# Performance work log

Measured on AMD Instinct MI355X. Metric: run time of the kernel, lower is better.

## Reference

```python
import jax, jax.numpy as jnp
import numpy as np

B, T, C = 8, 2048, 1024
H = 4 * C
N_LAYER, LAYER_ID = 12, 2
K_CLAMP = 60.0
LN_EPS = 1e-5


def _ln(x, g, b):
    m = jnp.mean(x, axis=-1, keepdims=True)
    v = jnp.var(x, axis=-1, keepdims=True)
    return (x - m) * jax.lax.rsqrt(v + LN_EPS) * g + b


def _mix(x, time_mix, combined_mix):
    # x: (B,T,C). Causal shift (zeros at t=0), anti-causal shift (zeros at t=T-1).
    c = x.shape[-1]
    xm1 = jnp.pad(x[:, :-1], ((0, 0), (1, 0), (0, 0)))
    xp1 = jnp.pad(x[:, 1:], ((0, 0), (0, 1), (0, 0)))
    xc = jnp.concatenate([xm1[..., :c // 2], xp1[..., c // 2:]], axis=-1)
    return x * time_mix + xm1 * (1.0 - time_mix) + xc * combined_mix


def _wkv(time_decay, time_first, k, v):
    # RWKV WKV exponential-decay linear recurrence (the custom CUDA kernel).
    # k, v: (B,T,C); k > 0 (already clamped+exp'd).
    # y_t = (a_t + exp(u)*k_t*v_t) / (b_t + exp(u)*k_t)
    # a_{t+1} = exp(-exp(w))*a_t + k_t*v_t ; b likewise with v=1.
    ed = jnp.exp(-jnp.exp(time_decay))  # per-step channel decay, (C,)
    eu = jnp.exp(time_first)            # current-token bonus, (C,)

    def step(carry, kv_t):
        a, b = carry
        kt, vt = kv_t
        y = (a + eu * kt * vt) / (b + eu * kt)
        return (ed * a + kt * vt, ed * b + kt), y

    kT = jnp.swapaxes(k, 0, 1)  # (T,B,C)
    vT = jnp.swapaxes(v, 0, 1)
    z = jnp.zeros_like(kT[0])
    _, y = jax.lax.scan(step, (z, z), (kT, vT))
    return jnp.swapaxes(y, 0, 1)  # (B,T,C)


def _time_mix_block(x, time_mix, combined_mix, time_decay, time_first, Wk, Wv, Wr, Wo):
    xm = _mix(x, time_mix, combined_mix)
    k = jnp.exp(jnp.minimum(xm @ Wk.T, K_CLAMP))
    v = xm @ Wv.T
    r = xm @ Wr.T
    wkv = _wkv(time_decay, time_first, k, v)
    return (jax.nn.sigmoid(r) * wkv) @ Wo.T


def _channel_mix_block(x, time_mix, combined_mix, Fk, Fv, Fr):
    xm = _mix(x, time_mix, combined_mix)
    k = jnp.square(jax.nn.relu(xm @ Fk.T))
    kv = k @ Fv.T
    return jax.nn.sigmoid(xm @ Fr.T) * kv


def setup_inputs():
    key = jax.random.key(0)
    ks = jax.random.split(key, 9)
    s = 0.02
    x = jax.random.normal(ks[0], (B, T, C), jnp.float32)
    # time_decay init per the module (f1/f2 interpolation over layers)
    h = np.arange(C, dtype=np.float64)
    frac = (LAYER_ID - 1) / (N_LAYER - 2)
    f1 = 3.0 + frac * (1.2 - 3.0)
    f2 = 0.65 + frac * (0.4 - 0.65)
    decay_speed = np.power(f2, h / (C - 1) * 7.0) * f1
    tm = jnp.concatenate([jnp.zeros(C // 2), jnp.ones(C // 2)]).reshape(1, 1, C).astype(jnp.float32)
    return dict(
        x=x,
        ln1_g=jnp.ones((C,), jnp.float32), ln1_b=jnp.zeros((C,), jnp.float32),
        ln2_g=jnp.ones((C,), jnp.float32), ln2_b=jnp.zeros((C,), jnp.float32),
        att_time_mix=tm,
        att_combined_mix=jnp.full((1, 1, C), 0.01, jnp.float32),
        time_decay=jnp.asarray(np.log(decay_speed), jnp.float32),
        time_first=jnp.full((C,), float(np.log(0.3)), jnp.float32),
        Wk=jax.random.normal(ks[1], (C, C), jnp.float32) * s,
        Wv=jax.random.normal(ks[2], (C, C), jnp.float32) * s,
        Wr=jax.random.normal(ks[3], (C, C), jnp.float32) * s,
        Wo=jax.random.normal(ks[4], (C, C), jnp.float32) * s,
        ffn_time_mix=tm,
        ffn_combined_mix=jnp.full((1, 1, C), 0.01, jnp.float32),
        Fk=jax.random.normal(ks[5], (H, C), jnp.float32) * s,
        Fv=jax.random.normal(ks[6], (C, H), jnp.float32) * s,
        Fr=jax.random.normal(ks[7], (C, C), jnp.float32) * s,
    )


def reference(x, ln1_g, ln1_b, ln2_g, ln2_b, att_time_mix, att_combined_mix,
              time_decay, time_first, Wk, Wv, Wr, Wo,
              ffn_time_mix, ffn_combined_mix, Fk, Fv, Fr):
    x = _ln(x, ln1_g, ln1_b)
    x = x + _time_mix_block(x, att_time_mix, att_combined_mix, time_decay, time_first, Wk, Wv, Wr, Wo)
    x = _ln(x, ln2_g, ln2_b)
    x = x + _channel_mix_block(x, ffn_time_mix, ffn_combined_mix, Fk, Fv, Fr)
    return x
```

## Files before the change

### kernel.cpp

```cpp
#include <hip/hip_runtime.h>
#include <hip/hip_bf16.h>

typedef float f32x4 __attribute__((ext_vector_type(4)));
typedef __bf16 bf16x8 __attribute__((ext_vector_type(8)));
typedef __bf16 bf16x4 __attribute__((ext_vector_type(4)));

#define DEVI static __device__ __forceinline__

DEVI void glds16(const void* g, void* l) {
  __builtin_amdgcn_global_load_lds((__attribute__((address_space(1))) void*)g,
                                   (__attribute__((address_space(3))) void*)l, 16, 0, 0);
}

DEVI f32x4 load4(const float* p) { return *(const f32x4*)p; }
DEVI f32x4 load4(const __bf16* p) {
  bf16x4 v = *(const bf16x4*)p;
  f32x4 o = { (float)v[0], (float)v[1], (float)v[2], (float)v[3] };
  return o;
}
DEVI void store4(float* p, f32x4 v) { *(f32x4*)p = v; }
DEVI void store4(__bf16* p, f32x4 v) {
  bf16x4 o = { (__bf16)v[0], (__bf16)v[1], (__bf16)v[2], (__bf16)v[3] };
  *(bf16x4*)p = o;
}

__global__ void cvt_bf16(const float* __restrict__ in, __bf16* __restrict__ out, int n4) {
  int i = blockIdx.x * 256 + threadIdx.x;
  if (i < n4) {
    f32x4 v = *(const f32x4*)(in + (size_t)i * 4);
    store4(out + (size_t)i * 4, v);
  }
}

template <typename TIN, typename TOUT>
__global__ __launch_bounds__(256) void ln_kernel(const TIN* __restrict__ x,
    const float* __restrict__ gw, const float* __restrict__ bw,
    TOUT* __restrict__ out) {
  const size_t row = blockIdx.x;
  f32x4 v = load4(x + row * 1024 + threadIdx.x * 4);
  float s = v[0] + v[1] + v[2] + v[3];
  float q = v[0]*v[0] + v[1]*v[1] + v[2]*v[2] + v[3]*v[3];
#pragma unroll
  for (int o = 32; o > 0; o >>= 1) { s += __shfl_down(s, o); q += __shfl_down(q, o); }
  __shared__ float ss[4], qq[4];
  const int w = threadIdx.x >> 6, l = threadIdx.x & 63;
  if (l == 0) { ss[w] = s; qq[w] = q; }
  __syncthreads();
  s = ss[0] + ss[1] + ss[2] + ss[3];
  q = qq[0] + qq[1] + qq[2] + qq[3];
  const float mean = s * (1.0f / 1024.0f);
  const float var = q * (1.0f / 1024.0f) - mean * mean;
  const float rstd = rsqrtf(var + 1e-5f);
  f32x4 g4 = *(const f32x4*)(gw + threadIdx.x * 4);
  f32x4 b4 = *(const f32x4*)(bw + threadIdx.x * 4);
  f32x4 o;
#pragma unroll
  for (int j = 0; j < 4; ++j) o[j] = (v[j] - mean) * rstd * g4[j] + b4[j];
  store4(out + row * 1024 + threadIdx.x * 4, o);
}

template <typename TIN>
__global__ __launch_bounds__(256) void mix_kernel(const TIN* __restrict__ x,
    const float* __restrict__ tm, const float* __restrict__ cm,
    __bf16* __restrict__ out) {
  const int idx = blockIdx.x * 256 + threadIdx.x;
  const int t = (idx >> 8) & 2047;
  const int c = (idx & 255) * 4;
  const size_t base = ((size_t)(idx >> 8) << 10) + c;
  f32x4 xv = load4(x + base);
  f32x4 xm1 = {0.f, 0.f, 0.f, 0.f}, xp1 = {0.f, 0.f, 0.f, 0.f};
  if (t > 0)    xm1 = load4(x + base - 1024);
  if (t < 2047) xp1 = load4(x + base + 1024);
  f32x4 tm4 = *(const f32x4*)(tm + c);
  f32x4 cm4 = *(const f32x4*)(cm + c);
  f32x4 xc = (c < 512) ? xm1 : xp1;
  f32x4 o;
#pragma unroll
  for (int j = 0; j < 4; ++j)
    o[j] = xv[j] * tm4[j] + xm1[j] * (1.0f - tm4[j]) + xc[j] * cm4[j];
  store4(out + base, o);
}

__global__ __launch_bounds__(256) void wkv_part(const __bf16* __restrict__ k,
    const __bf16* __restrict__ v, const float* __restrict__ td,
    float* __restrict__ scA, float* __restrict__ scB) {
  const int gid = blockIdx.x * 256 + threadIdx.x;
  const int c = gid & 1023;
  const int j = (gid >> 10) & 31;
  const int b = gid >> 15;
  const float ed = expf(-expf(td[c]));
  float A = 0.f, Bv = 0.f;
  size_t off = ((size_t)(b * 2048 + j * 64) << 10) + c;
#pragma unroll 4
  for (int i = 0; i < 64; ++i, off += 1024) {
    const float kt = (float)k[off];
    const float kv = kt * (float)v[off];
    A = ed * A + kv;
    Bv = ed * Bv + kt;
  }
  scA[gid] = A;
  scB[gid] = Bv;
}

__global__ __launch_bounds__(256) void wkv_scan(const float* __restrict__ td,
    float* __restrict__ scA, float* __restrict__ scB) {
  const int gid = blockIdx.x * 256 + threadIdx.x;
  const int c = gid & 1023;
  const int b = gid >> 10;
  const float edL = expf(-expf(td[c]) * 64.0f);
  float a = 0.f, bb = 0.f;
  size_t off = ((size_t)b << 15) + c;
  for (int j = 0; j < 32; ++j, off += 1024) {
    const float Aj = scA[off], Bj = scB[off];
    scA[off] = a;
    scB[off] = bb;
    a = edL * a + Aj;
    bb = edL * bb + Bj;
  }
}

__global__ __launch_bounds__(256) void wkv_apply(const __bf16* __restrict__ k,
    const __bf16* __restrict__ v, const __bf16* __restrict__ sr,
    const float* __restrict__ td, const float* __restrict__ tf,
    const float* __restrict__ scA, const float* __restrict__ scB,
    __bf16* __restrict__ srw) {
  const int gid = blockIdx.x * 256 + threadIdx.x;
  const int c = gid & 1023;
  const int j = (gid >> 10) & 31;
  const int b = gid >> 15;
  const float ed = expf(-expf(td[c]));
  const float eu = expf(tf[c]);
  float a = scA[gid], bb = scB[gid];
  size_t off = ((size_t)(b * 2048 + j * 64) << 10) + c;
#pragma unroll 4
  for (int i = 0; i < 64; ++i, off += 1024) {
    const float kt = (float)k[off];
    const float vt = (float)v[off];
    const float kv = kt * vt;
    const float y = (a + eu * kv) / (bb + eu * kt);
    srw[off] = (__bf16)((float)sr[off] * y);
    a = ed * a + kv;
    bb = ed * bb + kt;
  }
}

enum { EPI_NONE = 0, EPI_EXP, EPI_SIG, EPI_RELU2, EPI_RESID, EPI_FINAL, EPI_KVR };

#define SBAR() { __builtin_amdgcn_s_barrier(); __builtin_amdgcn_sched_barrier(0); }
#define WAITL0() { asm volatile("s_waitcnt lgkmcnt(0)" ::: "memory"); __builtin_amdgcn_sched_barrier(0); }
#define VMW(n) { asm volatile("s_waitcnt vmcnt(" #n ")" ::: "memory"); __builtin_amdgcn_sched_barrier(0); }

template <int EPI>
__global__ __launch_bounds__(512, 2) void gemm8p(
    const __bf16* __restrict__ A, const __bf16* __restrict__ W,
    void* outp, const void* res, const void* sig, const int N, const int K) {
  __shared__ __bf16 sA[2][16384];
  __shared__ __bf16 sB[2][16384];
  const int tid = threadIdx.x;
  const int w = tid >> 6, l = tid & 63;
  const int wm = w >> 2, wn = w & 3;

  const int nwg = gridDim.x * gridDim.y;
  int wg = blockIdx.y * gridDim.x + blockIdx.x;
  wg = (wg & 7) * (nwg >> 3) + (wg >> 3);
  const int m0 = (wg / gridDim.x) << 8;
  const int n0 = (wg % gridDim.x) << 8;

  const int lr = l >> 3;
  const int lc = (l & 7) ^ lr;
  const size_t gA = (size_t)(m0 + w * 8 + lr) * K + lc * 8;
  const size_t gB = (size_t)(n0 + wn * 64 + wm * 8 + lr) * K + lc * 8;
  const int ldsA = w * 512;
  const int ldsB = (wn * 64 + wm * 8) * 64;

  const int NTK = K >> 6;

#define STAGE_A(buf, kt, i) glds16(A + gA + (size_t)(i) * 64 * K + (size_t)(kt) * 64, &sA[buf][ldsA + (i) * 4096])
#define STAGE_B(buf, kt, j) glds16(W + gB + (size_t)(j) * 16 * K + (size_t)(kt) * 64, &sB[buf][ldsB + (j) * 1024])

  const int rA = (wm * 128 + (l & 15)) * 64;
  const int rB = (wn * 64 + (l & 15)) * 64;
  const int csw = l & 7;
  const int k0 = l >> 4;
#define LDA(buf, mi, kk) (*(const bf16x8*)&sA[buf][rA + (mi) * 1024 + ((((kk) * 4 + k0) ^ csw) << 3)])
#define LDB(buf, ni, kk) (*(const bf16x8*)&sB[buf][rB + (ni) * 1024 + ((((kk) * 4 + k0) ^ csw) << 3)])

  f32x4 acc[8][4] = {};
  bf16x8 afr[8], b0[4], b1[4];

  STAGE_B(0, 0, 0); STAGE_B(0, 0, 1); STAGE_A(0, 0, 0); STAGE_A(0, 0, 2);
  STAGE_B(0, 0, 2); STAGE_B(0, 0, 3); STAGE_A(0, 0, 1); STAGE_A(0, 0, 3);

  for (int kt = 0; kt < NTK; ++kt) {
    const int buf = kt & 1, nb = buf ^ 1;
    const bool st = (kt + 1 < NTK);
    VMW(4); SBAR();
#pragma unroll
    for (int mi = 0; mi < 4; ++mi) {
      afr[mi * 2 + 0] = LDA(buf, mi, 0);
      afr[mi * 2 + 1] = LDA(buf, mi, 1);
    }
#pragma unroll
    for (int ni = 0; ni < 2; ++ni) {
      b0[ni * 2 + 0] = LDB(buf, ni, 0);
      b0[ni * 2 + 1] = LDB(buf, ni, 1);
    }
    if (st) { STAGE_B(nb, kt + 1, 0); STAGE_B(nb, kt + 1, 1); }
    WAITL0();
    __builtin_amdgcn_s_setprio(1);
#pragma unroll
    for (int mi = 0; mi < 4; ++mi)
#pragma unroll
      for (int ni = 0; ni < 2; ++ni)
#pragma unroll
        for (int kk = 0; kk < 2; ++kk)
          acc[mi][ni] = __builtin_amdgcn_mfma_f32_16x16x32_bf16(afr[mi*2+kk], b0[ni*2+kk], acc[mi][ni], 0, 0, 0);
    __builtin_amdgcn_s_setprio(0);
    if (st) { VMW(4); } else { VMW(2); }
    SBAR();
#pragma unroll
    for (int ni = 0; ni < 2; ++ni) {
      b1[ni * 2 + 0] = LDB(buf, ni + 2, 0);
      b1[ni * 2 + 1] = LDB(buf, ni + 2, 1);
    }
    if (st) { STAGE_A(nb, kt + 1, 0); STAGE_A(nb, kt + 1, 2); }
    WAITL0();
    __builtin_amdgcn_s_setprio(1);
#pragma unroll
    for (int mi = 0; mi < 4; ++mi)
#pragma unroll
      for (int ni = 0; ni < 2; ++ni)
#pragma unroll
        for (int kk = 0; kk < 2; ++kk)
          acc[mi][ni + 2] = __builtin_amdgcn_mfma_f32_16x16x32_bf16(afr[mi*2+kk], b1[ni*2+kk], acc[mi][ni + 2], 0, 0, 0);
    __builtin_amdgcn_s_setprio(0);
    if (st) { VMW(4); } else { VMW(0); }
    SBAR();
#pragma unroll
    for (int mi = 0; mi < 4; ++mi) {
      afr[mi * 2 + 0] = LDA(buf, mi + 4, 0);
      afr[mi * 2 + 1] = LDA(buf, mi + 4, 1);
    }
    if (st) { STAGE_B(nb, kt + 1, 2); STAGE_B(nb, kt + 1, 3); }
    WAITL0();
    __builtin_amdgcn_s_setprio(1);
#pragma unroll
    for (int mi = 0; mi < 4; ++mi)
#pragma unroll
      for (int ni = 0; ni < 2; ++ni)
#pragma unroll
        for (int kk = 0; kk < 2; ++kk)
          acc[mi + 4][ni] = __builtin_amdgcn_mfma_f32_16x16x32_bf16(afr[mi*2+kk], b0[ni*2+kk], acc[mi + 4][ni], 0, 0, 0);
    __builtin_amdgcn_s_setprio(0);
    if (st) { STAGE_A(nb, kt + 1, 1); STAGE_A(nb, kt + 1, 3); }
    __builtin_amdgcn_s_setprio(1);
#pragma unroll
    for (int mi = 0; mi < 4; ++mi)
#pragma unroll
      for (int ni = 0; ni < 2; ++ni)
#pragma unroll
        for (int kk = 0; kk < 2; ++kk)
          acc[mi + 4][ni + 2] = __builtin_amdgcn_mfma_f32_16x16x32_bf16(afr[mi*2+kk], b1[ni*2+kk], acc[mi + 4][ni + 2], 0, 0, 0);
    __builtin_amdgcn_s_setprio(0);
  }

  const int rl = (l >> 4) << 2, cl = l & 15;
#pragma unroll
  for (int mi = 0; mi < 8; ++mi) {
#pragma unroll
    for (int ni = 0; ni < 4; ++ni) {
#pragma unroll
      for (int e = 0; e < 4; ++e) {
        const int r = m0 + (wm << 7) + mi * 16 + rl + e;
        const int cidx = n0 + (wn << 6) + ni * 16 + cl;
        const size_t idx = (size_t)r * N + cidx;
        const float vacc = acc[mi][ni][e];
        if constexpr (EPI == EPI_NONE) {
          ((__bf16*)outp)[idx] = (__bf16)vacc;
        } else if constexpr (EPI == EPI_EXP) {
          ((__bf16*)outp)[idx] = (__bf16)expf(fminf(vacc, 60.0f));
        } else if constexpr (EPI == EPI_SIG) {
          ((__bf16*)outp)[idx] = (__bf16)(1.0f / (1.0f + expf(-vacc)));
        } else if constexpr (EPI == EPI_RELU2) {
          const float rv = fmaxf(vacc, 0.0f);
          ((__bf16*)outp)[idx] = (__bf16)(rv * rv);
        } else if constexpr (EPI == EPI_RESID) {
          ((__bf16*)outp)[idx] = (__bf16)(vacc + (float)((const __bf16*)res)[idx]);
        } else if constexpr (EPI == EPI_FINAL) {
          ((float*)outp)[idx] = ((const float*)res)[idx] + (float)((const __bf16*)sig)[idx] * vacc;
        } else {
          const int sel = cidx >> 10;
          const size_t oidx = (size_t)r * 1024 + (cidx & 1023);
          if (sel == 0)      ((__bf16*)outp)[oidx] = (__bf16)expf(fminf(vacc, 60.0f));
          else if (sel == 1) ((__bf16*)const_cast<void*>(res))[oidx] = (__bf16)vacc;
          else               ((__bf16*)const_cast<void*>(sig))[oidx] = (__bf16)(1.0f / (1.0f + expf(-vacc)));
        }
      }
    }
  }
}

extern "C" void kernel_launch(void* const* d_in, const int* in_sizes, int n_in,
                              void* d_out, int out_size, void* d_ws, size_t ws_size,
                              hipStream_t stream) {
  (void)in_sizes; (void)n_in; (void)out_size;
  const float* x    = (const float*)d_in[0];
  const float* ln1g = (const float*)d_in[1];
  const float* ln1b = (const float*)d_in[2];
  const float* ln2g = (const float*)d_in[3];
  const float* ln2b = (const float*)d_in[4];
  const float* atm  = (const float*)d_in[5];
  const float* acm  = (const float*)d_in[6];
  const float* td   = (const float*)d_in[7];
  const float* tf   = (const float*)d_in[8];
  const float* Wk   = (const float*)d_in[9];
  const float* Wv   = (const float*)d_in[10];
  const float* Wr   = (const float*)d_in[11];
  const float* Wo   = (const float*)d_in[12];
  const float* ftm  = (const float*)d_in[13];
  const float* fcm  = (const float*)d_in[14];
  const float* Fk   = (const float*)d_in[15];
  const float* Fv   = (const float*)d_in[16];
  const float* Fr   = (const float*)d_in[17];

  constexpr size_t C = 1024, T = 2048, Bs = 8, H = 4096;
  constexpr size_t NT = Bs * T;
  constexpr size_t NTC = NT * C;
  constexpr size_t CC = C * C;
  constexpr size_t CH = C * H;

  char* p = (char*)d_ws;
  auto takeb = [&](size_t elems) { __bf16* q = (__bf16*)p; p += elems * 2; return q; };
  __bf16* wKVR = takeb(3 * CC);
  __bf16* wWo  = takeb(CC);
  __bf16* wFk  = takeb(CH);
  __bf16* wFv  = takeb(CH);
  __bf16* wFr  = takeb(CC);
  __bf16* Ab   = takeb(NTC);
  __bf16* Bb   = takeb(NTC);
  __bf16* Db   = takeb(NTC);
  float* scA = (float*)p; p += Bs * 32 * C * 4;
  float* scB = (float*)p; p += Bs * 32 * C * 4;
  __bf16* kk = (__bf16*)p;
  const size_t used = (size_t)(p - (char*)d_ws);
  const size_t kkcap = ws_size > used ? ws_size - used : 0;
  int chunks = 4;
  if (kkcap >= NT * H * 2)          chunks = 1;
  else if (kkcap >= NT * H)         chunks = 2;
  __bf16* Cb = kk;
  __bf16* sr  = (__bf16*)d_out;
  float*  x3  = (float*)d_out;

  auto cvt = [&](const float* src, size_t n, __bf16* dst) {
    const int n4 = (int)(n / 4);
    cvt_bf16<<<dim3((n4 + 255) / 256), dim3(256), 0, stream>>>(src, dst, n4);
  };
  cvt(Wk, CC, wKVR); cvt(Wv, CC, wKVR + CC); cvt(Wr, CC, wKVR + 2 * CC);
  cvt(Wo, CC, wWo); cvt(Fk, CH, wFk); cvt(Fv, CH, wFv); cvt(Fr, CC, wFr);

  const dim3 blk(256), blkG(512);

  ln_kernel<float, __bf16><<<dim3((unsigned)NT), blk, 0, stream>>>(x, ln1g, ln1b, Ab);
  mix_kernel<__bf16><<<dim3((unsigned)(NTC / 1024)), blk, 0, stream>>>(Ab, atm, acm, Bb);
  gemm8p<EPI_KVR><<<dim3(12, 64), blkG, 0, stream>>>(Bb, wKVR, Cb, Db, sr, 3072, 1024);
  wkv_part<<<dim3(1024), blk, 0, stream>>>(Cb, Db, td, scA, scB);
  wkv_scan<<<dim3(32), blk, 0, stream>>>(td, scA, scB);
  wkv_apply<<<dim3(1024), blk, 0, stream>>>(Cb, Db, sr, td, tf, scA, scB, Bb);
  gemm8p<EPI_RESID><<<dim3(4, 64), blkG, 0, stream>>>(Bb, wWo, Ab, Ab, nullptr, 1024, 1024);
  ln_kernel<__bf16, float><<<dim3((unsigned)NT), blk, 0, stream>>>(Ab, ln2g, ln2b, x3);
  mix_kernel<float><<<dim3((unsigned)(NTC / 1024)), blk, 0, stream>>>(x3, ftm, fcm, Db);
  gemm8p<EPI_SIG><<<dim3(4, 64), blkG, 0, stream>>>(Db, wFr, Bb, nullptr, nullptr, 1024, 1024);
  const size_t Mc = NT / chunks;
  for (int ch = 0; ch < chunks; ++ch) {
    const size_t ro = (size_t)ch * Mc;
    gemm8p<EPI_RELU2><<<dim3(16, (unsigned)(Mc / 256)), blkG, 0, stream>>>(
        Db + ro * C, wFk, kk, nullptr, nullptr, 4096, 1024);
    gemm8p<EPI_FINAL><<<dim3(4, (unsigned)(Mc / 256)), blkG, 0, stream>>>(
        kk, wFv, (float*)d_out + ro * C, (const float*)d_out + ro * C,
        Bb + ro * C, 1024, 4096);
  }
}
```

Before: 711.1 us.

## Reorder GEMM main loop to iterate k-halves outer with full-N fragments

Restructures the inner GEMM schedule so each phase loads four A fragments and all four B fragments for one k-half, then issues a 4x4 block of MFMAs. The old schedule split by N-halves and held eight A fragments. The new one uses fewer A registers and changes the ordering of global-to-LDS staging and vmcnt waits: all B tiles are staged first, then the A tiles. It aims to cut register pressure and improve the overlap of LDS reads with MFMAs. The trade-off is two barriers per iteration instead of three, and wait counts that must match the new staging order exactly.

```diff
diff --git a/kernel.cpp b/kernel.cpp
--- a/kernel.cpp
+++ b/kernel.cpp
@@ -186,81 +186,64 @@
 #define LDB(buf, ni, kk) (*(const bf16x8*)&sB[buf][rB + (ni) * 1024 + ((((kk) * 4 + k0) ^ csw) << 3)])
 
   f32x4 acc[8][4] = {};
-  bf16x8 afr[8], b0[4], b1[4];
-
-  STAGE_B(0, 0, 0); STAGE_B(0, 0, 1); STAGE_A(0, 0, 0); STAGE_A(0, 0, 2);
-  STAGE_B(0, 0, 2); STAGE_B(0, 0, 3); STAGE_A(0, 0, 1); STAGE_A(0, 0, 3);
+  bf16x8 a[4], b0[4], b1[4];
+
+  STAGE_B(0, 0, 0); STAGE_B(0, 0, 1); STAGE_B(0, 0, 2); STAGE_B(0, 0, 3);
+  STAGE_A(0, 0, 0); STAGE_A(0, 0, 2); STAGE_A(0, 0, 1); STAGE_A(0, 0, 3);
 
   for (int kt = 0; kt < NTK; ++kt) {
     const int buf = kt & 1, nb = buf ^ 1;
     const bool st = (kt + 1 < NTK);
-    VMW(4); SBAR();
-#pragma unroll
-    for (int mi = 0; mi < 4; ++mi) {
-      afr[mi * 2 + 0] = LDA(buf, mi, 0);
-      afr[mi * 2 + 1] = LDA(buf, mi, 1);
-    }
-#pragma unroll
-    for (int ni = 0; ni < 2; ++ni) {
-      b0[ni * 2 + 0] = LDB(buf, ni, 0);
-      b0[ni * 2 + 1] = LDB(buf, ni, 1);
-    }
+    VMW(2); SBAR();
     if (st) { STAGE_B(nb, kt + 1, 0); STAGE_B(nb, kt + 1, 1); }
+#pragma unroll
+    for (int i = 0; i < 4; ++i) a[i] = LDA(buf, i, 0);
+#pragma unroll
+    for (int i = 0; i < 4; ++i) b0[i] = LDB(buf, i, 0);
     WAITL0();
     __builtin_amdgcn_s_setprio(1);
 #pragma unroll
     for (int mi = 0; mi < 4; ++mi)
 #pragma unroll
-      for (int ni = 0; ni < 2; ++ni)
-#pragma unroll
-        for (int kk = 0; kk < 2; ++kk)
-          acc[mi][ni] = __builtin_amdgcn_mfma_f32_16x16x32_bf16(afr[mi*2+kk], b0[ni*2+kk], acc[mi][ni], 0, 0, 0);
+      for (int ni = 0; ni < 4; ++ni)
+        acc[mi][ni] = __builtin_amdgcn_mfma_f32_16x16x32_bf16(a[mi], b0[ni], acc[mi][ni], 0, 0, 0);
     __builtin_amdgcn_s_setprio(0);
-    if (st) { VMW(4); } else { VMW(2); }
+    if (st) { VMW(2); } else { VMW(0); }
     SBAR();
-#pragma unroll
-    for (int ni = 0; ni < 2; ++ni) {
-      b1[ni * 2 + 0] = LDB(buf, ni + 2, 0);
-      b1[ni * 2 + 1] = LDB(buf, ni + 2, 1);
-    }
-    if (st) { STAGE_A(nb, kt + 1, 0); STAGE_A(nb, kt + 1, 2); }
+    if (st) { STAGE_B(nb, kt + 1, 2); STAGE_B(nb, kt + 1, 3); }
+#pragma unroll
+    for (int i = 0; i < 4; ++i) a[i] = LDA(buf, i + 4, 0);
     WAITL0();
     __builtin_amdgcn_s_setprio(1);
 #pragma unroll
     for (int mi = 0; mi < 4; ++mi)
 #pragma unroll
-      for (int ni = 0; ni < 2; ++ni)
-#pragma unroll
-        for (int kk = 0; kk < 2; ++kk)
-          acc[mi][ni + 2] = __builtin_amdgcn_mfma_f32_16x16x32_bf16(afr[mi*2+kk], b1[ni*2+kk], acc[mi][ni + 2], 0, 0, 0);
+      for (int ni = 0; ni < 4; ++ni)
+        acc[mi + 4][ni] = __builtin_amdgcn_mfma_f32_16x16x32_bf16(a[mi], b0[ni], acc[mi + 4][ni], 0, 0, 0);
     __builtin_amdgcn_s_setprio(0);
-    if (st) { VMW(4); } else { VMW(0); }
-    SBAR();
-#pragma unroll
-    for (int mi = 0; mi < 4; ++mi) {
-      afr[mi * 2 + 0] = LDA(buf, mi + 4, 0);
-      afr[mi * 2 + 1] = LDA(buf, mi + 4, 1);
-    }
-    if (st) { STAGE_B(nb, kt + 1, 2); STAGE_B(nb, kt + 1, 3); }
+    if (st) { STAGE_A(nb, kt + 1, 0); STAGE_A(nb, kt + 1, 2); }
+#pragma unroll
+    for (int i = 0; i < 4; ++i) a[i] = LDA(buf, i, 1);
+#pragma unroll
+    for (int i = 0; i < 4; ++i) b1[i] = LDB(buf, i, 1);
     WAITL0();
     __builtin_amdgcn_s_setprio(1);
 #pragma unroll
     for (int mi = 0; mi < 4; ++mi)
 #pragma unroll
-      for (int ni = 0; ni < 2; ++ni)
-#pragma unroll
-        for (int kk = 0; kk < 2; ++kk)
-          acc[mi + 4][ni] = __builtin_amdgcn_mfma_f32_16x16x32_bf16(afr[mi*2+kk], b0[ni*2+kk], acc[mi + 4][ni], 0, 0, 0);
+      for (int ni = 0; ni < 4; ++ni)
+        acc[mi][ni] = __builtin_amdgcn_mfma_f32_16x16x32_bf16(a[mi], b1[ni], acc[mi][ni], 0, 0, 0);
     __builtin_amdgcn_s_setprio(0);
     if (st) { STAGE_A(nb, kt + 1, 1); STAGE_A(nb, kt + 1, 3); }
+#pragma unroll
+    for (int i = 0; i < 4; ++i) a[i] = LDA(buf, i + 4, 1);
+    WAITL0();
     __builtin_amdgcn_s_setprio(1);
 #pragma unroll
     for (int mi = 0; mi < 4; ++mi)
 #pragma unroll
-      for (int ni = 0; ni < 2; ++ni)
-#pragma unroll
-        for (int kk = 0; kk < 2; ++kk)
-          acc[mi + 4][ni + 2] = __builtin_amdgcn_mfma_f32_16x16x32_bf16(afr[mi*2+kk], b1[ni*2+kk], acc[mi + 4][ni + 2], 0, 0, 0);
+      for (int ni = 0; ni < 4; ++ni)
+        acc[mi + 4][ni] = __builtin_amdgcn_mfma_f32_16x16x32_bf16(a[mi], b1[ni], acc[mi + 4][ni], 0, 0, 0);
     __builtin_amdgcn_s_setprio(0);
   }
 
```

New measurement: 836.9 us. 1.18x slower.

## Fuse Fk/Fr GEMMs, merge weight conversions, vectorize WKV kernels by four channels

Applied to the files above, without the earlier changes.

Concatenates the Fk and Fr weights so the channel-mix key and receptance projections run as one GEMM with a split epilogue. All seven weight conversions are merged into a single kernel writing a contiguous bf16 buffer. The WKV part/scan/apply kernels now process four channels per thread with vector loads and stores. This reduces launches and memory transactions, but it cuts the thread count of the latency-bound recurrence kernels by four.

```diff
diff --git a/kernel.cpp b/kernel.cpp
--- a/kernel.cpp
+++ b/kernel.cpp
@@ -24,12 +24,28 @@
   *(bf16x4*)p = o;
 }
 
-__global__ void cvt_bf16(const float* __restrict__ in, __bf16* __restrict__ out, int n4) {
-  int i = blockIdx.x * 256 + threadIdx.x;
-  if (i < n4) {
-    f32x4 v = *(const f32x4*)(in + (size_t)i * 4);
-    store4(out + (size_t)i * 4, v);
-  }
+constexpr size_t C = 1024, T = 2048, Bs = 8, H = 4096;
+constexpr size_t NT = Bs * T;
+constexpr size_t NTC = NT * C;
+constexpr size_t CC = C * C;
+constexpr size_t CH = C * H;
+
+__global__ __launch_bounds__(256) void cvt_all(
+    const float* __restrict__ Wk, const float* __restrict__ Wv,
+    const float* __restrict__ Wr, const float* __restrict__ Wo,
+    const float* __restrict__ Fk, const float* __restrict__ Fr,
+    const float* __restrict__ Fv, __bf16* __restrict__ out) {
+  const size_t e = ((size_t)blockIdx.x * 256 + threadIdx.x) * 4;
+  const float* src; size_t rel;
+  if      (e < CC)                   { src = Wk; rel = e; }
+  else if (e < 2 * CC)               { src = Wv; rel = e - CC; }
+  else if (e < 3 * CC)               { src = Wr; rel = e - 2 * CC; }
+  else if (e < 4 * CC)               { src = Wo; rel = e - 3 * CC; }
+  else if (e < 4 * CC + CH)          { src = Fk; rel = e - 4 * CC; }
+  else if (e < 5 * CC + CH)          { src = Fr; rel = e - 4 * CC - CH; }
+  else                               { src = Fv; rel = e - 5 * CC - CH; }
+  f32x4 v = *(const f32x4*)(src + rel);
+  store4(out + e, v);
 }
 
 template <typename TIN, typename TOUT>
@@ -85,37 +101,51 @@
     const __bf16* __restrict__ v, const float* __restrict__ td,
     float* __restrict__ scA, float* __restrict__ scB) {
   const int gid = blockIdx.x * 256 + threadIdx.x;
-  const int c = gid & 1023;
-  const int j = (gid >> 10) & 31;
-  const int b = gid >> 15;
-  const float ed = expf(-expf(td[c]));
-  float A = 0.f, Bv = 0.f;
+  const int c = (gid & 255) * 4;
+  const int j = (gid >> 8) & 31;
+  const int b = gid >> 13;
+  float ed[4], A[4] = {}, Bv[4] = {};
+#pragma unroll
+  for (int q = 0; q < 4; ++q) ed[q] = expf(-expf(td[c + q]));
   size_t off = ((size_t)(b * 2048 + j * 64) << 10) + c;
-#pragma unroll 4
   for (int i = 0; i < 64; ++i, off += 1024) {
-    const float kt = (float)k[off];
-    const float kv = kt * (float)v[off];
-    A = ed * A + kv;
-    Bv = ed * Bv + kt;
-  }
-  scA[gid] = A;
-  scB[gid] = Bv;
+    bf16x4 k4 = *(const bf16x4*)(k + off);
+    bf16x4 v4 = *(const bf16x4*)(v + off);
+#pragma unroll
+    for (int q = 0; q < 4; ++q) {
+      const float kt = (float)k4[q];
+      A[q] = ed[q] * A[q] + kt * (float)v4[q];
+      Bv[q] = ed[q] * Bv[q] + kt;
+    }
+  }
+  const size_t sidx = (((size_t)b * 32 + j) << 10) + c;
+  f32x4 oA = { A[0], A[1], A[2], A[3] };
+  f32x4 oB = { Bv[0], Bv[1], Bv[2], Bv[3] };
+  *(f32x4*)(scA + sidx) = oA;
+  *(f32x4*)(scB + sidx) = oB;
 }
 
 __global__ __launch_bounds__(256) void wkv_scan(const float* __restrict__ td,
     float* __restrict__ scA, float* __restrict__ scB) {
   const int gid = blockIdx.x * 256 + threadIdx.x;
-  const int c = gid & 1023;
-  const int b = gid >> 10;
-  const float edL = expf(-expf(td[c]) * 64.0f);
-  float a = 0.f, bb = 0.f;
+  const int c = (gid & 255) * 4;
+  const int b = gid >> 8;
+  float edL[4], a[4] = {}, bb[4] = {};
+#pragma unroll
+  for (int q = 0; q < 4; ++q) edL[q] = expf(-expf(td[c + q]) * 64.0f);
   size_t off = ((size_t)b << 15) + c;
   for (int j = 0; j < 32; ++j, off += 1024) {
-    const float Aj = scA[off], Bj = scB[off];
-    scA[off] = a;
-    scB[off] = bb;
-    a = edL * a + Aj;
-    bb = edL * bb + Bj;
+    f32x4 Aj = *(const f32x4*)(scA + off);
+    f32x4 Bj = *(const f32x4*)(scB + off);
+    f32x4 ca = { a[0], a[1], a[2], a[3] };
+    f32x4 cb = { bb[0], bb[1], bb[2], bb[3] };
+    *(f32x4*)(scA + off) = ca;
+    *(f32x4*)(scB + off) = cb;
+#pragma unroll
+    for (int q = 0; q < 4; ++q) {
+      a[q] = edL[q] * a[q] + Aj[q];
+      bb[q] = edL[q] * bb[q] + Bj[q];
+    }
   }
 }
 
@@ -125,26 +155,37 @@
     const float* __restrict__ scA, const float* __restrict__ scB,
     __bf16* __restrict__ srw) {
   const int gid = blockIdx.x * 256 + threadIdx.x;
-  const int c = gid & 1023;
-  const int j = (gid >> 10) & 31;
-  const int b = gid >> 15;
-  const float ed = expf(-expf(td[c]));
-  const float eu = expf(tf[c]);
-  float a = scA[gid], bb = scB[gid];
+  const int c = (gid & 255) * 4;
+  const int j = (gid >> 8) & 31;
+  const int b = gid >> 13;
+  float ed[4], eu[4], a[4], bb[4];
+#pragma unroll
+  for (int q = 0; q < 4; ++q) { ed[q] = expf(-expf(td[c + q])); eu[q] = expf(tf[c + q]); }
+  const size_t sidx = (((size_t)b * 32 + j) << 10) + c;
+  f32x4 ca = *(const f32x4*)(scA + sidx);
+  f32x4 cb = *(const f32x4*)(scB + sidx);
+#pragma unroll
+  for (int q = 0; q < 4; ++q) { a[q] = ca[q]; bb[q] = cb[q]; }
   size_t off = ((size_t)(b * 2048 + j * 64) << 10) + c;
-#pragma unroll 4
   for (int i = 0; i < 64; ++i, off += 1024) {
-    const float kt = (float)k[off];
-    const float vt = (float)v[off];
-    const float kv = kt * vt;
-    const float y = (a + eu * kv) / (bb + eu * kt);
-    srw[off] = (__bf16)((float)sr[off] * y);
-    a = ed * a + kv;
-    bb = ed * bb + kt;
-  }
-}
-
-enum { EPI_NONE = 0, EPI_EXP, EPI_SIG, EPI_RELU2, EPI_RESID, EPI_FINAL, EPI_KVR };
+    bf16x4 k4 = *(const bf16x4*)(k + off);
+    bf16x4 v4 = *(const bf16x4*)(v + off);
+    bf16x4 s4 = *(const bf16x4*)(sr + off);
+    bf16x4 o4;
+#pragma unroll
+    for (int q = 0; q < 4; ++q) {
+      const float kt = (float)k4[q];
+      const float kv = kt * (float)v4[q];
+      const float y = (a[q] + eu[q] * kv) / (bb[q] + eu[q] * kt);
+      o4[q] = (__bf16)((float)s4[q] * y);
+      a[q] = ed[q] * a[q] + kv;
+      bb[q] = ed[q] * bb[q] + kt;
+    }
+    *(bf16x4*)(srw + off) = o4;
+  }
+}
+
+enum { EPI_RESID = 0, EPI_FINAL, EPI_KVR, EPI_FKR };
 
 #define SBAR() { __builtin_amdgcn_s_barrier(); __builtin_amdgcn_sched_barrier(0); }
 #define WAITL0() { asm volatile("s_waitcnt lgkmcnt(0)" ::: "memory"); __builtin_amdgcn_sched_barrier(0); }
@@ -273,27 +314,27 @@
       for (int e = 0; e < 4; ++e) {
         const int r = m0 + (wm << 7) + mi * 16 + rl + e;
         const int cidx = n0 + (wn << 6) + ni * 16 + cl;
-        const size_t idx = (size_t)r * N + cidx;
         const float vacc = acc[mi][ni][e];
-        if constexpr (EPI == EPI_NONE) {
-          ((__bf16*)outp)[idx] = (__bf16)vacc;
-        } else if constexpr (EPI == EPI_EXP) {
-          ((__bf16*)outp)[idx] = (__bf16)expf(fminf(vacc, 60.0f));
-        } else if constexpr (EPI == EPI_SIG) {
-          ((__bf16*)outp)[idx] = (__bf16)(1.0f / (1.0f + expf(-vacc)));
-        } else if constexpr (EPI == EPI_RELU2) {
-          const float rv = fmaxf(vacc, 0.0f);
-          ((__bf16*)outp)[idx] = (__bf16)(rv * rv);
-        } else if constexpr (EPI == EPI_RESID) {
+        if constexpr (EPI == EPI_RESID) {
+          const size_t idx = (size_t)r * 1024 + cidx;
           ((__bf16*)outp)[idx] = (__bf16)(vacc + (float)((const __bf16*)res)[idx]);
         } else if constexpr (EPI == EPI_FINAL) {
+          const size_t idx = (size_t)r * 1024 + cidx;
           ((float*)outp)[idx] = ((const float*)res)[idx] + (float)((const __bf16*)sig)[idx] * vacc;
-        } else {
+        } else if constexpr (EPI == EPI_KVR) {
           const int sel = cidx >> 10;
           const size_t oidx = (size_t)r * 1024 + (cidx & 1023);
           if (sel == 0)      ((__bf16*)outp)[oidx] = (__bf16)expf(fminf(vacc, 60.0f));
           else if (sel == 1) ((__bf16*)const_cast<void*>(res))[oidx] = (__bf16)vacc;
           else               ((__bf16*)const_cast<void*>(sig))[oidx] = (__bf16)(1.0f / (1.0f + expf(-vacc)));
+        } else {
+          if ((cidx >> 12) == 0) {
+            const float rv = fmaxf(vacc, 0.0f);
+            ((__bf16*)outp)[(size_t)r * 4096 + cidx] = (__bf16)(rv * rv);
+          } else {
+            ((__bf16*)const_cast<void*>(sig))[(size_t)r * 1024 + (cidx - 4096)] =
+                (__bf16)(1.0f / (1.0f + expf(-vacc)));
+          }
         }
       }
     }
@@ -323,19 +364,12 @@
   const float* Fv   = (const float*)d_in[16];
   const float* Fr   = (const float*)d_in[17];
 
-  constexpr size_t C = 1024, T = 2048, Bs = 8, H = 4096;
-  constexpr size_t NT = Bs * T;
-  constexpr size_t NTC = NT * C;
-  constexpr size_t CC = C * C;
-  constexpr size_t CH = C * H;
-
   char* p = (char*)d_ws;
   auto takeb = [&](size_t elems) { __bf16* q = (__bf16*)p; p += elems * 2; return q; };
   __bf16* wKVR = takeb(3 * CC);
   __bf16* wWo  = takeb(CC);
-  __bf16* wFk  = takeb(CH);
+  __bf16* wFKR = takeb(CH + CC);
   __bf16* wFv  = takeb(CH);
-  __bf16* wFr  = takeb(CC);
   __bf16* Ab   = takeb(NTC);
   __bf16* Bb   = takeb(NTC);
   __bf16* Db   = takeb(NTC);
@@ -351,30 +385,25 @@
   __bf16* sr  = (__bf16*)d_out;
   float*  x3  = (float*)d_out;
 
-  auto cvt = [&](const float* src, size_t n, __bf16* dst) {
-    const int n4 = (int)(n / 4);
-    cvt_bf16<<<dim3((n4 + 255) / 256), dim3(256), 0, stream>>>(src, dst, n4);
-  };
-  cvt(Wk, CC, wKVR); cvt(Wv, CC, wKVR + CC); cvt(Wr, CC, wKVR + 2 * CC);
-  cvt(Wo, CC, wWo); cvt(Fk, CH, wFk); cvt(Fv, CH, wFv); cvt(Fr, CC, wFr);
-
   const dim3 blk(256), blkG(512);
+
+  cvt_all<<<dim3((unsigned)((5 * CC + 2 * CH) / 4 / 256)), blk, 0, stream>>>(
+      Wk, Wv, Wr, Wo, Fk, Fr, Fv, wKVR);
 
   ln_kernel<float, __bf16><<<dim3((unsigned)NT), blk, 0, stream>>>(x, ln1g, ln1b, Ab);
   mix_kernel<__bf16><<<dim3((unsigned)(NTC / 1024)), blk, 0, stream>>>(Ab, atm, acm, Bb);
   gemm8p<EPI_KVR><<<dim3(12, 64), blkG, 0, stream>>>(Bb, wKVR, Cb, Db, sr, 3072, 1024);
-  wkv_part<<<dim3(1024), blk, 0, stream>>>(Cb, Db, td, scA, scB);
-  wkv_scan<<<dim3(32), blk, 0, stream>>>(td, scA, scB);
-  wkv_apply<<<dim3(1024), blk, 0, stream>>>(Cb, Db, sr, td, tf, scA, scB, Bb);
+  wkv_part<<<dim3(256), blk, 0, stream>>>(Cb, Db, td, scA, scB);
+  wkv_scan<<<dim3(8), blk, 0, stream>>>(td, scA, scB);
+  wkv_apply<<<dim3(256), blk, 0, stream>>>(Cb, Db, sr, td, tf, scA, scB, Bb);
   gemm8p<EPI_RESID><<<dim3(4, 64), blkG, 0, stream>>>(Bb, wWo, Ab, Ab, nullptr, 1024, 1024);
   ln_kernel<__bf16, float><<<dim3((unsigned)NT), blk, 0, stream>>>(Ab, ln2g, ln2b, x3);
   mix_kernel<float><<<dim3((unsigned)(NTC / 1024)), blk, 0, stream>>>(x3, ftm, fcm, Db);
-  gemm8p<EPI_SIG><<<dim3(4, 64), blkG, 0, stream>>>(Db, wFr, Bb, nullptr, nullptr, 1024, 1024);
   const size_t Mc = NT / chunks;
   for (int ch = 0; ch < chunks; ++ch) {
     const size_t ro = (size_t)ch * Mc;
-    gemm8p<EPI_RELU2><<<dim3(16, (unsigned)(Mc / 256)), blkG, 0, stream>>>(
-        Db + ro * C, wFk, kk, nullptr, nullptr, 4096, 1024);
+    gemm8p<EPI_FKR><<<dim3(20, (unsigned)(Mc / 256)), blkG, 0, stream>>>(
+        Db + ro * C, wFKR, kk, nullptr, Bb + ro * C, 5120, 1024);
     gemm8p<EPI_FINAL><<<dim3(4, (unsigned)(Mc / 256)), blkG, 0, stream>>>(
         kk, wFv, (float*)d_out + ro * C, (const float*)d_out + ro * C,
         Bb + ro * C, 1024, 4096);
```

Result: slower. 736.3 us (+3.5%).
